# Performance work log

Measured on AMD Instinct MI355X. Metric: run time of the kernel, lower is better.

The kernel has to match this reference:

```python
import jax, jax.numpy as jnp
import numpy as np
import math

INF = 1e10

def setup_inputs() -> dict:
    key = jax.random.key(0)
    ks = jax.random.split(key, 6)
    B, S, T, D = 8, 1024, 1024, 1024
    stdv = 1.0 / math.sqrt(D)
    return {
        "key": jax.random.normal(ks[0], (B, S, D), dtype=jnp.float32),
        "mask_src": jnp.ones((B, S), dtype=jnp.float32),
        "mask_trg": jnp.ones((B, T), dtype=jnp.float32),
        "Wq": jax.random.uniform(ks[1], (D, D), jnp.float32, -stdv, stdv),
        "bq": jnp.zeros((D,), jnp.float32),
        "Wk": jax.random.uniform(ks[2], (D, D), jnp.float32, -stdv, stdv),
        "bk": jnp.zeros((D,), jnp.float32),
        "wg": jax.random.uniform(ks[3], (D,), jnp.float32, -stdv, stdv),
        "bg": jnp.zeros((1,), jnp.float32),
    }


def reference(key, mask_src, mask_trg, Wq, bq, Wk, bk, wg, bg):
    B, S, D = key.shape
    T = mask_trg.shape[1]
    scale = jnp.asarray(math.sqrt(D), key.dtype)

    # --- linear (position-based Gaussian) attention ---
    src_lens = mask_src.sum(-1)                      # [B]
    trg_lens = mask_trg.sum(-1)                      # [B]
    steps = src_lens / trg_lens                      # [B]
    idx_t = steps[:, None] * jnp.arange(T, dtype=key.dtype)[None, :]   # [B,T]
    idx_s = jnp.arange(S, dtype=key.dtype)                              # [S]
    dist2 = (idx_s[None, None, :] - idx_t[:, :, None]) ** 2            # [B,T,S]
    l_logits = -dist2 / 0.3 - INF * (1.0 - mask_src[:, None, :])
    l_att = jax.nn.softmax(l_logits, axis=-1)                           # [B,T,S]

    # query from position attention
    query = jnp.einsum('bts,bsd->btd', l_att, key)                      # [B,T,D]

    # learned gate, broadcast [B,T,1] -> [B,T,S]
    gates = jax.nn.sigmoid(query @ wg + bg)[:, :, None]                 # [B,T,1]

    # QK dot-product attention
    q = query @ Wq.T + bq                                               # [B,T,D]
    k = key @ Wk.T + bk                                                 # [B,S,D]
    dots = jnp.einsum('btd,bsd->bts', q, k)
    dots = dots - (1.0 - mask_src[:, None, :]) * INF
    probs = jax.nn.softmax(dots / scale, axis=-1)                       # [B,T,S]

    # gated mixture of QK attention and position attention
    return (1.0 - gates) * probs + gates * l_att
```

## Files before the change

### kernel.cpp

```cpp
#include <hip/hip_runtime.h>
#include <hip/hip_bf16.h>
#include <stdint.h>

typedef unsigned short ushort_t;

#define BB 8
#define SS 1024
#define TT 1024
#define DD 1024
#define INF_ 1e10f

__device__ __forceinline__ float b2f(ushort_t u){
  union { unsigned u32; float f; } x; x.u32 = ((unsigned)u) << 16; return x.f;
}
__device__ __forceinline__ ushort_t f2b(float f){
  union { float f; unsigned u; } x; x.f = f;
  unsigned r = x.u + 0x7FFFu + ((x.u >> 16) & 1u);
  return (ushort_t)(r >> 16);
}

__global__ __launch_bounds__(256) void steps_kernel(
    const float* __restrict__ msrc, const float* __restrict__ mtrg,
    float* __restrict__ steps, float* __restrict__ v2)
{
  __shared__ float sh[8];
  int b = blockIdx.x, tid = threadIdx.x;
  if (b < 4) v2[b*256 + tid] = 0.f;
  float a = 0.f, c = 0.f;
  for (int i = tid; i < SS; i += 256) a += msrc[b*SS + i];
  for (int i = tid; i < TT; i += 256) c += mtrg[b*TT + i];
  #pragma unroll
  for (int o = 32; o; o >>= 1){ a += __shfl_xor(a, o); c += __shfl_xor(c, o); }
  int wv = tid >> 6, ln = tid & 63;
  if (!ln){ sh[wv] = a; sh[4+wv] = c; }
  __syncthreads();
  if (!tid){
    float sa = sh[0]+sh[1]+sh[2]+sh[3];
    float sc = sh[4]+sh[5]+sh[6]+sh[7];
    steps[b] = sa / sc;
  }
}

__global__ __launch_bounds__(256) void v2_kernel(
    const float* __restrict__ Wk, const float* __restrict__ bq,
    float* __restrict__ v2)
{
  int tid = threadIdx.x;
  int f = tid * 4;
  int r0 = blockIdx.x * 32;
  float a0=0.f, a1=0.f, a2=0.f, a3=0.f;
  for (int r = 0; r < 32; r++){
    float s = bq[r0 + r];
    float4 w = *(const float4*)(Wk + (size_t)(r0 + r)*DD + f);
    a0 += s*w.x; a1 += s*w.y; a2 += s*w.z; a3 += s*w.w;
  }
  atomicAdd(&v2[f+0], a0); atomicAdd(&v2[f+1], a1);
  atomicAdd(&v2[f+2], a2); atomicAdd(&v2[f+3], a3);
}

__global__ __launch_bounds__(256) void key_convert_kernel(
    const float* __restrict__ key, const float* __restrict__ wg,
    const float* __restrict__ v2f, ushort_t* __restrict__ keyb,
    float* __restrict__ kw, float* __restrict__ cv)
{
  __shared__ float sh[8];
  int row = blockIdx.x;
  int tid = threadIdx.x, d0 = tid*4;
  float4 v = *(const float4*)(key + (size_t)row*DD + d0);
  ushort4 o; o.x=f2b(v.x); o.y=f2b(v.y); o.z=f2b(v.z); o.w=f2b(v.w);
  *(ushort4*)(keyb + (size_t)row*DD + d0) = o;
  float4 w4 = *(const float4*)(wg + d0);
  float4 u4 = *(const float4*)(v2f + d0);
  float pk = v.x*w4.x + v.y*w4.y + v.z*w4.z + v.w*w4.w;
  float pc = v.x*u4.x + v.y*u4.y + v.z*u4.z + v.w*u4.w;
  #pragma unroll
  for (int off = 32; off; off >>= 1){ pk += __shfl_xor(pk, off); pc += __shfl_xor(pc, off); }
  int wvv = tid >> 6;
  if ((tid & 63) == 0){ sh[wvv] = pk; sh[4+wvv] = pc; }
  __syncthreads();
  if (!tid){
    kw[row] = sh[0]+sh[1]+sh[2]+sh[3];
    cv[row] = sh[4]+sh[5]+sh[6]+sh[7];
  }
}

__global__ __launch_bounds__(256) void transpose_convert_kernel(
    const float* __restrict__ src, ushort_t* __restrict__ dst)
{
  __shared__ float tile[32][33];
  int tx = blockIdx.x, ty = blockIdx.y;
  int tid = threadIdx.x;
  int c = tid & 31, r0 = tid >> 5;
  #pragma unroll
  for (int k = 0; k < 4; k++){
    int r = r0 + k*8;
    tile[r][c] = src[(size_t)(ty*32 + r)*DD + tx*32 + c];
  }
  __syncthreads();
  #pragma unroll
  for (int k = 0; k < 4; k++){
    int r = r0 + k*8;
    dst[(size_t)(tx*32 + r)*DD + ty*32 + c] = f2b(tile[c][r]);
  }
}

typedef __bf16 bf16x8 __attribute__((ext_vector_type(8)));
typedef float f32x4 __attribute__((ext_vector_type(4)));

#define CP16(g, l) __builtin_amdgcn_global_load_lds( \
    (const __attribute__((address_space(1))) void*)(g), \
    (__attribute__((address_space(3))) void*)(l), 16, 0, 0)

__global__ __launch_bounds__(256, 2) void gemm_bt_kernel(
    const ushort_t* __restrict__ A, const ushort_t* __restrict__ Bm,
    const float* __restrict__ bias, void* __restrict__ Cv,
    int M, int N, int K, int lda, int ldb,
    long long sA, long long sB, long long sC, int hasBias, int outBF16,
    int gx, int gxy)
{
  __shared__ ushort_t lA[128*32];
  __shared__ ushort_t lB[128*32];

  const int bpx = gridDim.x >> 3;
  const int lin = blockIdx.x;
  const int glob = (lin & 7) * bpx + (lin >> 3);
  const int bz = glob / gxy;
  const int rem = glob - bz * gxy;
  const int by = rem / gx;
  const int bx = rem - by * gx;

  A  += (size_t)bz * sA;
  Bm += (size_t)bz * sB;

  const int tid = threadIdx.x;
  const int wv = tid >> 6, ln = tid & 63;
  const int r4 = ln >> 2, c8 = (ln & 3) * 8;

  const ushort_t* gA0 = A  + (size_t)(by*128 + wv*32 + r4) * lda + c8;
  const ushort_t* gA1 = gA0 + (size_t)16 * lda;
  const ushort_t* gB0 = Bm + (size_t)(bx*128 + wv*32 + r4) * ldb + c8;
  const ushort_t* gB1 = gB0 + (size_t)16 * ldb;
  ushort_t* lA0 = &lA[(wv*32     ) * 32];
  ushort_t* lA1 = &lA[(wv*32 + 16) * 32];
  ushort_t* lB0 = &lB[(wv*32     ) * 32];
  ushort_t* lB1 = &lB[(wv*32 + 16) * 32];

  const int lm = ln & 15, qd = ln >> 4;
  const int wm = (wv >> 1) * 64, wn = (wv & 1) * 64;

  f32x4 acc[4][4];
  #pragma unroll
  for (int i = 0; i < 4; i++)
    #pragma unroll
    for (int j = 0; j < 4; j++) acc[i][j] = (f32x4){0.f, 0.f, 0.f, 0.f};

  for (int k0 = 0; k0 < K; k0 += 32){
    CP16(gA0, lA0); CP16(gA1, lA1); CP16(gB0, lB0); CP16(gB1, lB1);
    gA0 += 32; gA1 += 32; gB0 += 32; gB1 += 32;
    __syncthreads();
    bf16x8 af[4], bf[4];
    #pragma unroll
    for (int i = 0; i < 4; i++) af[i] = *(const bf16x8*)&lA[(wm + i*16 + lm)*32 + qd*8];
    #pragma unroll
    for (int j = 0; j < 4; j++) bf[j] = *(const bf16x8*)&lB[(wn + j*16 + lm)*32 + qd*8];
    #pragma unroll
    for (int i = 0; i < 4; i++)
      #pragma unroll
      for (int j = 0; j < 4; j++)
        acc[i][j] = __builtin_amdgcn_mfma_f32_16x16x32_bf16(af[i], bf[j], acc[i][j], 0, 0, 0);
    __syncthreads();
  }

  const int row0 = by*128 + wm + qd*4;
  const int col0 = bx*128 + wn + lm;
  ushort_t* Cb = (ushort_t*)Cv + (size_t)bz * sC;
  float*    Cf = (float*)Cv    + (size_t)bz * sC;
  #pragma unroll
  for (int j = 0; j < 4; j++){
    int col = col0 + j*16;
    float bv = hasBias ? bias[col] : 0.f;
    #pragma unroll
    for (int i = 0; i < 4; i++)
      #pragma unroll
      for (int r = 0; r < 4; r++){
        size_t idx = (size_t)(row0 + i*16 + r) * N + col;
        float v = acc[i][j][r] + bv;
        if (outBF16) Cb[idx] = f2b(v); else Cf[idx] = v;
      }
  }
}

__global__ __launch_bounds__(256) void wmt_reduce_kernel(
    const float* __restrict__ part, ushort_t* __restrict__ dst)
{
  int i4 = blockIdx.x * 256 + threadIdx.x;
  const float4* p = (const float4*)part;
  float4 a = p[i4];
  float4 b = p[i4 + 262144];
  float4 c = p[i4 + 524288];
  float4 d = p[i4 + 786432];
  ushort4 o;
  o.x = f2b(a.x + b.x + c.x + d.x);
  o.y = f2b(a.y + b.y + c.y + d.y);
  o.z = f2b(a.z + b.z + c.z + d.z);
  o.w = f2b(a.w + b.w + c.w + d.w);
  ((ushort4*)dst)[i4] = o;
}

__global__ __launch_bounds__(256) void band_kernel(
    const ushort_t* __restrict__ kmb, const float* __restrict__ mask_src,
    const float* __restrict__ steps, const float* __restrict__ kw,
    const float* __restrict__ bg, ushort_t* __restrict__ qm2b,
    float* __restrict__ gates)
{
  __shared__ float shw[8][17];
  __shared__ int shslo[8];
  int bx = blockIdx.x;
  int b = bx >> 7, t0 = (bx & 127) * 8;
  int tid = threadIdx.x;

  if (tid < 8){
    int t = t0 + tid;
    float c = steps[b] * (float)t;
    int slo = (int)ceilf(c - 8.0f);
    float w[17], m = -3e38f;
    #pragma unroll
    for (int i = 0; i < 17; i++){
      int s = slo + i;
      float l = -3e38f;
      if (s >= 0 && s < SS){
        float dd = (float)s - c;
        l = -dd*dd*(1.0f/0.3f) - INF_*(1.0f - mask_src[b*SS + s]);
      }
      w[i] = l; m = fmaxf(m, l);
    }
    float norm = 0.f, ga = 0.f;
    #pragma unroll
    for (int i = 0; i < 17; i++){
      float e = __expf(w[i] - m);
      int s = slo + i;
      if (s >= 0 && s < SS) ga += e * kw[b*SS + s]; else e = 0.f;
      w[i] = e; norm += e;
    }
    float inv = 1.0f / norm;
    #pragma unroll
    for (int i = 0; i < 17; i++) shw[tid][i] = w[i] * inv;
    shslo[tid] = slo;
    gates[b*TT + t] = 1.0f / (1.0f + __expf(-(ga*inv + bg[0])));
  }
  __syncthreads();

  int smin = shslo[0], smax = shslo[7] + 16;
  if (smin < 0) smin = 0;
  if (smax > SS-1) smax = SS-1;
  int d0 = tid * 4;
  float acc[8][4];
  #pragma unroll
  for (int t = 0; t < 8; t++){ acc[t][0]=0.f; acc[t][1]=0.f; acc[t][2]=0.f; acc[t][3]=0.f; }

  const ushort_t* kbase = kmb + ((size_t)b*SS)*DD + d0;
  for (int s = smin; s <= smax; s++){
    ushort4 kv = *(const ushort4*)(kbase + (size_t)s*DD);
    float k0 = b2f(kv.x), k1 = b2f(kv.y), k2 = b2f(kv.z), k3 = b2f(kv.w);
    #pragma unroll
    for (int t = 0; t < 8; t++){
      unsigned u = (unsigned)(s - shslo[t]);
      if (u < 17u){
        float wgt = shw[t][u];
        acc[t][0] += wgt*k0; acc[t][1] += wgt*k1; acc[t][2] += wgt*k2; acc[t][3] += wgt*k3;
      }
    }
  }
  #pragma unroll
  for (int t = 0; t < 8; t++){
    ushort4 o; o.x=f2b(acc[t][0]); o.y=f2b(acc[t][1]); o.z=f2b(acc[t][2]); o.w=f2b(acc[t][3]);
    *(ushort4*)(qm2b + ((size_t)(b*TT + t0 + t))*DD + d0) = o;
  }
}

__device__ __forceinline__ float blkmax(float v, float* sh){
  #pragma unroll
  for (int o = 32; o; o >>= 1) v = fmaxf(v, __shfl_xor(v, o));
  __syncthreads();
  if ((threadIdx.x & 63) == 0) sh[threadIdx.x >> 6] = v;
  __syncthreads();
  return fmaxf(fmaxf(sh[0], sh[1]), fmaxf(sh[2], sh[3]));
}
__device__ __forceinline__ float blksum(float v, float* sh){
  #pragma unroll
  for (int o = 32; o; o >>= 1) v += __shfl_xor(v, o);
  __syncthreads();
  if ((threadIdx.x & 63) == 0) sh[threadIdx.x >> 6] = v;
  __syncthreads();
  return sh[0] + sh[1] + sh[2] + sh[3];
}

__global__ __launch_bounds__(256) void softmax_mix_kernel(
    float* __restrict__ dots_out, const float* __restrict__ mask_src,
    const float* __restrict__ steps, const float* __restrict__ gates,
    const float* __restrict__ cv)
{
  __shared__ float sh[4];
  int blk = blockIdx.x;
  int b = blk >> 10, t = blk & 1023;
  int tid = threadIdx.x;
  int s0 = tid * 4;
  float c = steps[b] * (float)t;

  float4 dv = *(const float4*)(dots_out + (size_t)blk*SS + s0);
  float4 mv = *(const float4*)(mask_src + (size_t)b*SS + s0);
  float4 cva = *(const float4*)(cv + (size_t)b*SS + s0);
  float dvf[4] = {dv.x + cva.x, dv.y + cva.y, dv.z + cva.z, dv.w + cva.w};
  float msk[4] = {mv.x, mv.y, mv.z, mv.w};
  float dl[4], ll[4];
  float dmax = -3e38f, lmax = -3e38f;
  #pragma unroll
  for (int r = 0; r < 4; r++){
    float im = INF_ * (1.0f - msk[r]);
    dl[r] = (dvf[r] - im) * (1.0f/32.0f);
    float dd = (float)(s0 + r) - c;
    ll[r] = -dd*dd*(1.0f/0.3f) - im;
    dmax = fmaxf(dmax, dl[r]);
    lmax = fmaxf(lmax, ll[r]);
  }
  float dm = blkmax(dmax, sh);
  float ps[4], lp[4];
  float psum = 0.f, lsum = 0.f;
  #pragma unroll
  for (int r = 0; r < 4; r++){ ps[r] = __expf(dl[r] - dm); psum += ps[r]; }
  psum = blksum(psum, sh);
  float lm2 = blkmax(lmax, sh);
  #pragma unroll
  for (int r = 0; r < 4; r++){ lp[r] = __expf(ll[r] - lm2); lsum += lp[r]; }
  lsum = blksum(lsum, sh);

  float g = gates[blk];
  float ip = (1.0f - g) / psum, il = g / lsum;
  float4 ov;
  ov.x = ps[0]*ip + lp[0]*il;
  ov.y = ps[1]*ip + lp[1]*il;
  ov.z = ps[2]*ip + lp[2]*il;
  ov.w = ps[3]*ip + lp[3]*il;
  *(float4*)(dots_out + (size_t)blk*SS + s0) = ov;
}

extern "C" void kernel_launch(void* const* d_in, const int* in_sizes, int n_in,
                              void* d_out, int out_size, void* d_ws, size_t ws_size,
                              hipStream_t stream)
{
  const float* key      = (const float*)d_in[0];
  const float* mask_src = (const float*)d_in[1];
  const float* mask_trg = (const float*)d_in[2];
  const float* Wq       = (const float*)d_in[3];
  const float* bq       = (const float*)d_in[4];
  const float* Wk       = (const float*)d_in[5];
  const float* bk       = (const float*)d_in[6];
  const float* wg       = (const float*)d_in[7];
  const float* bg       = (const float*)d_in[8];
  float* out = (float*)d_out;
  (void)bk;

  char* ws = (char*)d_ws;
  float* steps     = (float*)ws;
  float* gates     = (float*)(ws + 4096);
  float* cv        = (float*)(ws + 4096 + 32768);
  float* kw        = (float*)(ws + 4096 + 65536);
  float* v2        = (float*)(ws + 4096 + 98304);
  ushort_t* WqTb   = (ushort_t*)(ws + 131072);
  ushort_t* WkTb   = WqTb + (size_t)DD*DD;
  ushort_t* WmTb   = WkTb + (size_t)DD*DD;
  ushort_t* keyb   = WmTb + (size_t)DD*DD;
  ushort_t* kmb    = keyb + (size_t)BB*SS*DD;
  char* shared16   = (char*)(kmb + (size_t)BB*SS*DD);
  float* wmPart    = (float*)shared16;
  ushort_t* qm2b   = (ushort_t*)shared16;

  steps_kernel<<<BB, 256, 0, stream>>>(mask_src, mask_trg, steps, v2);
  v2_kernel<<<32, 256, 0, stream>>>(Wk, bq, v2);
  key_convert_kernel<<<BB*SS, 256, 0, stream>>>(key, wg, v2, keyb, kw, cv);
  transpose_convert_kernel<<<dim3(32,32), 256, 0, stream>>>(Wq, WqTb);
  transpose_convert_kernel<<<dim3(32,32), 256, 0, stream>>>(Wk, WkTb);
  gemm_bt_kernel<<<256, 256, 0, stream>>>(
      WkTb, WqTb, nullptr, (void*)wmPart, DD, DD, DD/4, DD, DD,
      DD/4, DD/4, (long long)DD*DD, 0, 0, 8, 64);
  wmt_reduce_kernel<<<DD*DD/4/256, 256, 0, stream>>>(wmPart, WmTb);
  gemm_bt_kernel<<<512, 256, 0, stream>>>(
      keyb, WmTb, nullptr, (void*)kmb, BB*SS, DD, DD, DD, DD, 0, 0, 0, 0, 1, 8, 512);
  band_kernel<<<BB*TT/8, 256, 0, stream>>>(kmb, mask_src, steps, kw, bg, qm2b, gates);
  gemm_bt_kernel<<<512, 256, 0, stream>>>(
      qm2b, keyb, nullptr, (void*)out, TT, SS, DD, DD, DD,
      (long long)TT*DD, (long long)SS*DD, (long long)TT*SS, 0, 0, 8, 64);
  softmax_mix_kernel<<<BB*TT, 256, 0, stream>>>(out, mask_src, steps, gates, cv);
}
```

Before: 223.0 us.

## Store QK dot scores as bf16 and merge preprocessing launches

The final dot-product GEMM now writes its scores in bf16 into a reused workspace buffer (kmb) instead of fp32 into the output. The softmax-mix kernel reads those bf16 scores and writes fp32 results to the output, which halves the traffic for that intermediate. The two weight transpose-convert launches and the steps kernel are also merged into a single pre_kernel launch to cut launch overhead. Rounding the logits to bf16 before the softmax adds error, since the scores are scaled by 1/32 before exponentiation.

```diff
diff --git a/kernel.cpp b/kernel.cpp
--- a/kernel.cpp
+++ b/kernel.cpp
@@ -19,25 +19,48 @@
   return (ushort_t)(r >> 16);
 }
 
-__global__ __launch_bounds__(256) void steps_kernel(
+__global__ __launch_bounds__(256) void pre_kernel(
+    const float* __restrict__ Wq, const float* __restrict__ Wk,
+    ushort_t* __restrict__ WqT, ushort_t* __restrict__ WkT,
     const float* __restrict__ msrc, const float* __restrict__ mtrg,
     float* __restrict__ steps, float* __restrict__ v2)
 {
+  __shared__ float tile[32][33];
   __shared__ float sh[8];
-  int b = blockIdx.x, tid = threadIdx.x;
-  if (b < 4) v2[b*256 + tid] = 0.f;
-  float a = 0.f, c = 0.f;
-  for (int i = tid; i < SS; i += 256) a += msrc[b*SS + i];
-  for (int i = tid; i < TT; i += 256) c += mtrg[b*TT + i];
-  #pragma unroll
-  for (int o = 32; o; o >>= 1){ a += __shfl_xor(a, o); c += __shfl_xor(c, o); }
-  int wv = tid >> 6, ln = tid & 63;
-  if (!ln){ sh[wv] = a; sh[4+wv] = c; }
-  __syncthreads();
-  if (!tid){
-    float sa = sh[0]+sh[1]+sh[2]+sh[3];
-    float sc = sh[4]+sh[5]+sh[6]+sh[7];
-    steps[b] = sa / sc;
+  int blk = blockIdx.x, tid = threadIdx.x;
+  if (blk < 2048){
+    const float* src = (blk >= 1024) ? Wk : Wq;
+    ushort_t* dst = (blk >= 1024) ? WkT : WqT;
+    int q = blk & 1023;
+    int tx = q & 31, ty = q >> 5;
+    int c = tid & 31, r0 = tid >> 5;
+    #pragma unroll
+    for (int k = 0; k < 4; k++){
+      int r = r0 + k*8;
+      tile[r][c] = src[(size_t)(ty*32 + r)*DD + tx*32 + c];
+    }
+    __syncthreads();
+    #pragma unroll
+    for (int k = 0; k < 4; k++){
+      int r = r0 + k*8;
+      dst[(size_t)(tx*32 + r)*DD + ty*32 + c] = f2b(tile[c][r]);
+    }
+  } else {
+    int b = blk - 2048;
+    if (b < 4) v2[b*256 + tid] = 0.f;
+    float a = 0.f, c = 0.f;
+    for (int i = tid; i < SS; i += 256) a += msrc[b*SS + i];
+    for (int i = tid; i < TT; i += 256) c += mtrg[b*TT + i];
+    #pragma unroll
+    for (int o = 32; o; o >>= 1){ a += __shfl_xor(a, o); c += __shfl_xor(c, o); }
+    int wv = tid >> 6, ln = tid & 63;
+    if (!ln){ sh[wv] = a; sh[4+wv] = c; }
+    __syncthreads();
+    if (!tid){
+      float sa = sh[0]+sh[1]+sh[2]+sh[3];
+      float sc = sh[4]+sh[5]+sh[6]+sh[7];
+      steps[b] = sa / sc;
+    }
   }
 }
 
@@ -81,26 +104,6 @@
   if (!tid){
     kw[row] = sh[0]+sh[1]+sh[2]+sh[3];
     cv[row] = sh[4]+sh[5]+sh[6]+sh[7];
-  }
-}
-
-__global__ __launch_bounds__(256) void transpose_convert_kernel(
-    const float* __restrict__ src, ushort_t* __restrict__ dst)
-{
-  __shared__ float tile[32][33];
-  int tx = blockIdx.x, ty = blockIdx.y;
-  int tid = threadIdx.x;
-  int c = tid & 31, r0 = tid >> 5;
-  #pragma unroll
-  for (int k = 0; k < 4; k++){
-    int r = r0 + k*8;
-    tile[r][c] = src[(size_t)(ty*32 + r)*DD + tx*32 + c];
-  }
-  __syncthreads();
-  #pragma unroll
-  for (int k = 0; k < 4; k++){
-    int r = r0 + k*8;
-    dst[(size_t)(tx*32 + r)*DD + ty*32 + c] = f2b(tile[c][r]);
   }
 }
 
@@ -296,9 +299,9 @@
 }
 
 __global__ __launch_bounds__(256) void softmax_mix_kernel(
-    float* __restrict__ dots_out, const float* __restrict__ mask_src,
-    const float* __restrict__ steps, const float* __restrict__ gates,
-    const float* __restrict__ cv)
+    const ushort_t* __restrict__ dotsb, float* __restrict__ out,
+    const float* __restrict__ mask_src, const float* __restrict__ steps,
+    const float* __restrict__ gates, const float* __restrict__ cv)
 {
   __shared__ float sh[4];
   int blk = blockIdx.x;
@@ -307,10 +310,10 @@
   int s0 = tid * 4;
   float c = steps[b] * (float)t;
 
-  float4 dv = *(const float4*)(dots_out + (size_t)blk*SS + s0);
+  ushort4 dv = *(const ushort4*)(dotsb + (size_t)blk*SS + s0);
   float4 mv = *(const float4*)(mask_src + (size_t)b*SS + s0);
   float4 cva = *(const float4*)(cv + (size_t)b*SS + s0);
-  float dvf[4] = {dv.x + cva.x, dv.y + cva.y, dv.z + cva.z, dv.w + cva.w};
+  float dvf[4] = {b2f(dv.x) + cva.x, b2f(dv.y) + cva.y, b2f(dv.z) + cva.z, b2f(dv.w) + cva.w};
   float msk[4] = {mv.x, mv.y, mv.z, mv.w};
   float dl[4], ll[4];
   float dmax = -3e38f, lmax = -3e38f;
@@ -341,7 +344,7 @@
   ov.y = ps[1]*ip + lp[1]*il;
   ov.z = ps[2]*ip + lp[2]*il;
   ov.w = ps[3]*ip + lp[3]*il;
-  *(float4*)(dots_out + (size_t)blk*SS + s0) = ov;
+  *(float4*)(out + (size_t)blk*SS + s0) = ov;
 }
 
 extern "C" void kernel_launch(void* const* d_in, const int* in_sizes, int n_in,
@@ -374,12 +377,11 @@
   char* shared16   = (char*)(kmb + (size_t)BB*SS*DD);
   float* wmPart    = (float*)shared16;
   ushort_t* qm2b   = (ushort_t*)shared16;
-
-  steps_kernel<<<BB, 256, 0, stream>>>(mask_src, mask_trg, steps, v2);
+  ushort_t* dotsb  = kmb;
+
+  pre_kernel<<<2056, 256, 0, stream>>>(Wq, Wk, WqTb, WkTb, mask_src, mask_trg, steps, v2);
   v2_kernel<<<32, 256, 0, stream>>>(Wk, bq, v2);
   key_convert_kernel<<<BB*SS, 256, 0, stream>>>(key, wg, v2, keyb, kw, cv);
-  transpose_convert_kernel<<<dim3(32,32), 256, 0, stream>>>(Wq, WqTb);
-  transpose_convert_kernel<<<dim3(32,32), 256, 0, stream>>>(Wk, WkTb);
   gemm_bt_kernel<<<256, 256, 0, stream>>>(
       WkTb, WqTb, nullptr, (void*)wmPart, DD, DD, DD/4, DD, DD,
       DD/4, DD/4, (long long)DD*DD, 0, 0, 8, 64);
@@ -388,7 +390,7 @@
       keyb, WmTb, nullptr, (void*)kmb, BB*SS, DD, DD, DD, DD, 0, 0, 0, 0, 1, 8, 512);
   band_kernel<<<BB*TT/8, 256, 0, stream>>>(kmb, mask_src, steps, kw, bg, qm2b, gates);
   gemm_bt_kernel<<<512, 256, 0, stream>>>(
-      qm2b, keyb, nullptr, (void*)out, TT, SS, DD, DD, DD,
-      (long long)TT*DD, (long long)SS*DD, (long long)TT*SS, 0, 0, 8, 64);
-  softmax_mix_kernel<<<BB*TT, 256, 0, stream>>>(out, mask_src, steps, gates, cv);
-}
+      qm2b, keyb, nullptr, (void*)dotsb, TT, SS, DD, DD, DD,
+      (long long)TT*DD, (long long)SS*DD, (long long)TT*SS, 0, 1, 8, 64);
+  softmax_mix_kernel<<<BB*TT, 256, 0, stream>>>(dotsb, out, mask_src, steps, gates, cv);
+}
```

Measured after the change: 217.1 us. 2.6% less time.
